# Performance work log

Hardware: AMD Instinct MI355X
Metric: run time of the kernel (lower is better)

## Reference

```python
import jax, jax.numpy as jnp
import numpy as np

N = 8192
D = 256

def setup_inputs() -> dict:
    key = jax.random.key(0)
    k1, k2, k3 = jax.random.split(key, 3)
    x = jax.random.normal(k1, (N, D), dtype=jnp.float32)
    adj_matrix = jax.random.uniform(k2, (N, N), dtype=jnp.float32)
    weight = jax.random.normal(k3, (D, D), dtype=jnp.float32) * 0.02
    bias = jnp.zeros((D,), dtype=jnp.float32)
    return {"x": x, "adj_matrix": adj_matrix, "weight": weight, "bias": bias}

def reference(x, adj_matrix, weight, bias):
    # degree = row sums of adjacency
    degree = jnp.sum(adj_matrix, axis=1)  # [N]
    inv_deg = 1.0 / degree               # inverse of diagonal degree matrix
    # D^-1 @ A @ D^-1 == A scaled by inv_deg on rows and columns
    normalized_adj = adj_matrix * inv_deg[:, None] * inv_deg[None, :]  # [N,N]
    h = jnp.matmul(normalized_adj, x)          # [N,D] aggregation
    h = jnp.matmul(h, weight) + bias           # [N,D] transform
    return jax.nn.relu(h)
```

## Files before the change

kernel.cpp:

```cpp
#include <hip/hip_runtime.h>
#include <stdint.h>
#include <stdio.h>

#define NROWS 8192
#define DDIM 256

typedef __attribute__((ext_vector_type(8))) __bf16 bf16x8;
typedef __attribute__((ext_vector_type(4))) float f32x4;
typedef __attribute__((address_space(3))) uint32_t as3u32;
typedef __attribute__((address_space(1))) uint32_t as1u32;

__device__ __forceinline__ void glds16(const void* g, void* l) {
  __builtin_amdgcn_global_load_lds((const as1u32*)g, (as3u32*)l, 16, 0, 0);
}

__device__ __forceinline__ ushort f2b(float f) {
  uint32_t u = __float_as_uint(f);
  return (ushort)((u + 0x7FFFu + ((u >> 16) & 1u)) >> 16);
}

__global__ __launch_bounds__(256) void degree_cast_kernel(const float* __restrict__ A,
                                                          ushort* __restrict__ Ab,
                                                          float* __restrict__ inv_deg) {
  const int row = blockIdx.x * 4 + (threadIdx.x >> 6);
  const int lane = threadIdx.x & 63;
  const float4* r4 = (const float4*)(A + (size_t)row * NROWS);
  ushort* wr = Ab + (size_t)row * NROWS;
  float s = 0.f;
#pragma unroll
  for (int i = 0; i < 32; ++i) {
    float4 v = r4[lane + (i << 6)];
    s += (v.x + v.y) + (v.z + v.w);
    ushort4 b;
    b.x = f2b(v.x); b.y = f2b(v.y); b.z = f2b(v.z); b.w = f2b(v.w);
    *(ushort4*)(wr + (size_t)(lane + (i << 6)) * 4) = b;
  }
#pragma unroll
  for (int o = 32; o > 0; o >>= 1) s += __shfl_xor(s, o, 64);
  if (lane == 0) inv_deg[row] = 1.0f / s;
}

__global__ __launch_bounds__(256) void transpose_scale_kernel(const float* __restrict__ src,
                                                              const float* __restrict__ scale,
                                                              ushort* __restrict__ dst, int K) {
  __shared__ ushort tile[64 * 256];
  const int k0 = blockIdx.x * 64;
  const int w = threadIdx.x >> 6;
  const int lane = threadIdx.x & 63;
#pragma unroll
  for (int i = 0; i < 16; ++i) {
    const int r = w * 16 + i;
    float4 v = *(const float4*)(src + (size_t)(k0 + r) * DDIM + lane * 4);
    const float sc = scale ? scale[k0 + r] : 1.0f;
    ushort4 b;
    b.x = f2b(v.x * sc); b.y = f2b(v.y * sc);
    b.z = f2b(v.z * sc); b.w = f2b(v.w * sc);
    *(ushort4*)&tile[r * 256 + lane * 4] = b;
  }
  __syncthreads();
  const int c = threadIdx.x;
  ushort* drow = dst + (size_t)c * K + k0;
#pragma unroll
  for (int s = 0; s < 8; ++s) {
    uint32_t p[4];
#pragma unroll
    for (int j = 0; j < 4; ++j) {
      uint32_t lo = tile[(s * 8 + 2 * j + 0) * 256 + c];
      uint32_t hi = tile[(s * 8 + 2 * j + 1) * 256 + c];
      p[j] = lo | (hi << 16);
    }
    uint4 u; u.x = p[0]; u.y = p[1]; u.z = p[2]; u.w = p[3];
    *(uint4*)(drow + s * 8) = u;
  }
}

__global__ __launch_bounds__(512, 2) void gemm_big_kernel(
    const ushort* __restrict__ Ab,
    const ushort* __restrict__ Bt,
    const float* __restrict__ rowscale,
    float* __restrict__ Cpart) {
  __shared__ ushort Asm[2][128 * 64];
  __shared__ ushort Bsm[2][256 * 64];

  const int tid = threadIdx.x;
  const int lane = tid & 63;
  const int w = tid >> 6;
  const int wm = w >> 2;
  const int wn = w & 3;

  const int ks = blockIdx.x & 3;
  const int mb = blockIdx.x >> 2;
  const int m0 = mb * 128;
  const size_t kstart = (size_t)ks * 2048;

  const int al_r = lane >> 3;
  const int al_c = lane & 7;
  const int asw = al_c ^ al_r;
  const char* agA = (const char*)(Ab + (size_t)(m0 + 16 * w + al_r) * NROWS + kstart) + asw * 16;
  const char* bgB = (const char*)(Bt + (size_t)(32 * w + al_r) * NROWS + kstart) + asw * 16;
  const size_t grp = (size_t)8 * NROWS * 2;

  const int fr = lane & 15;
  const int q = lane >> 4;
  const int fsw = fr & 7;

  f32x4 acc[4][4] = {};
  const int NT = 2048 / 64;

  {
    glds16(agA, &Asm[0][(16 * w + 0) * 64]);
    glds16(agA + grp, &Asm[0][(16 * w + 8) * 64]);
#pragma unroll
    for (int j = 0; j < 4; ++j)
      glds16(bgB + (size_t)j * grp, &Bsm[0][(32 * w + 8 * j) * 64]);
  }

  int cur = 0;
  for (int t = 0; t < NT; ++t) {
    __syncthreads();
    if (t + 1 < NT) {
      const size_t koff = (size_t)(t + 1) * 128;
      glds16(agA + koff, &Asm[cur ^ 1][(16 * w + 0) * 64]);
      glds16(agA + grp + koff, &Asm[cur ^ 1][(16 * w + 8) * 64]);
#pragma unroll
      for (int j = 0; j < 4; ++j)
        glds16(bgB + (size_t)j * grp + koff, &Bsm[cur ^ 1][(32 * w + 8 * j) * 64]);
    }
#pragma unroll
    for (int kk = 0; kk < 2; ++kk) {
      uint4 af[4], bfr[4];
#pragma unroll
      for (int m = 0; m < 4; ++m)
        af[m] = *(const uint4*)((const char*)&Asm[cur][0] +
                 ((64 * wm + 16 * m + fr) * 128 + (((4 * kk + q) ^ fsw) << 4)));
#pragma unroll
      for (int n = 0; n < 4; ++n)
        bfr[n] = *(const uint4*)((const char*)&Bsm[cur][0] +
                 ((64 * wn + 16 * n + fr) * 128 + (((4 * kk + q) ^ fsw) << 4)));
#pragma unroll
      for (int m = 0; m < 4; ++m)
#pragma unroll
        for (int n = 0; n < 4; ++n)
          acc[m][n] = __builtin_amdgcn_mfma_f32_16x16x32_bf16(
              __builtin_bit_cast(bf16x8, af[m]), __builtin_bit_cast(bf16x8, bfr[n]),
              acc[m][n], 0, 0, 0);
    }
    cur ^= 1;
  }

  float* Cp = Cpart + (size_t)ks * ((size_t)NROWS * DDIM);
#pragma unroll
  for (int m = 0; m < 4; ++m)
#pragma unroll
    for (int r = 0; r < 4; ++r) {
      const int row = m0 + 64 * wm + 16 * m + q * 4 + r;
      const float sc = rowscale[row];
#pragma unroll
      for (int n = 0; n < 4; ++n) {
        const int col = 64 * wn + 16 * n + fr;
        Cp[(size_t)row * DDIM + col] = acc[m][n][r] * sc;
      }
    }
}

__global__ __launch_bounds__(512, 4) void gemm_small_kernel(
    const float* __restrict__ Hp, int npart, size_t pstride,
    const ushort* __restrict__ Bt,
    const float* __restrict__ bias, float* __restrict__ C) {
  const int K = DDIM;
  __shared__ ushort Asm[2][32 * 32];
  __shared__ ushort Bsm[2][256 * 32];

  const int tid = threadIdx.x;
  const int lane = tid & 63;
  const int w = tid >> 6;
  const int m0 = blockIdx.x * 32;

  f32x4 acc[2][2] = {};
  const int NT = K >> 5;

  const int arow = tid >> 3;
  const int aseg = tid & 7;
  const float* ag = Hp + (size_t)(m0 + arow) * DDIM + aseg * 4;
  const int awoff = arow * 32 + ((((aseg >> 1) ^ ((arow >> 1) & 3)) << 3) | ((aseg & 1) << 2));

  const int bch0 = w * 2;
  const int bq = lane >> 2;
  const int bswz = (lane & 3) ^ ((lane >> 3) & 3);
  const char* bg0 = (const char*)Bt + (size_t)(bch0 * 16 + bq) * ((size_t)K * 2) + bswz * 16;
  const char* bg1 = bg0 + (size_t)16 * ((size_t)K * 2);

  const int fr = lane & 15;
  const int fsw = (fr >> 1) & 3;
  const int fch = (lane >> 4) ^ fsw;
  const int aoff0 = fr * 32 + (fch << 3);
  const int aoff1 = (16 + fr) * 32 + (fch << 3);
  const int boff0 = (w * 32 + fr) * 32 + (fch << 3);
  const int boff1 = (w * 32 + 16 + fr) * 32 + (fch << 3);

  auto loadA = [&](int t) {
    float4 v; v.x = v.y = v.z = v.w = 0.f;
    for (int p = 0; p < npart; ++p) {
      float4 u = *(const float4*)(ag + (size_t)p * pstride + t * 32);
      v.x += u.x; v.y += u.y; v.z += u.z; v.w += u.w;
    }
    return v;
  };

  if (tid < 256) {
    float4 v = loadA(0);
    ushort4 b; b.x = f2b(v.x); b.y = f2b(v.y); b.z = f2b(v.z); b.w = f2b(v.w);
    *(ushort4*)&Asm[0][awoff] = b;
  }
  glds16(bg0, &Bsm[0][(bch0 + 0) * 512]);
  glds16(bg1, &Bsm[0][(bch0 + 1) * 512]);

  int cur = 0;
  for (int t = 0; t < NT; ++t) {
    __syncthreads();
    const bool pf = (t + 1 < NT);
    float4 av;
    if (pf) {
      if (tid < 256) av = loadA(t + 1);
      glds16(bg0 + (size_t)(t + 1) * 64, &Bsm[cur ^ 1][(bch0 + 0) * 512]);
      glds16(bg1 + (size_t)(t + 1) * 64, &Bsm[cur ^ 1][(bch0 + 1) * 512]);
    }
    uint4 a0 = *(const uint4*)&Asm[cur][aoff0];
    uint4 a1 = *(const uint4*)&Asm[cur][aoff1];
    uint4 b0 = *(const uint4*)&Bsm[cur][boff0];
    uint4 b1 = *(const uint4*)&Bsm[cur][boff1];
    acc[0][0] = __builtin_amdgcn_mfma_f32_16x16x32_bf16(
        __builtin_bit_cast(bf16x8, a0), __builtin_bit_cast(bf16x8, b0), acc[0][0], 0, 0, 0);
    acc[0][1] = __builtin_amdgcn_mfma_f32_16x16x32_bf16(
        __builtin_bit_cast(bf16x8, a0), __builtin_bit_cast(bf16x8, b1), acc[0][1], 0, 0, 0);
    acc[1][0] = __builtin_amdgcn_mfma_f32_16x16x32_bf16(
        __builtin_bit_cast(bf16x8, a1), __builtin_bit_cast(bf16x8, b0), acc[1][0], 0, 0, 0);
    acc[1][1] = __builtin_amdgcn_mfma_f32_16x16x32_bf16(
        __builtin_bit_cast(bf16x8, a1), __builtin_bit_cast(bf16x8, b1), acc[1][1], 0, 0, 0);
    if (pf && tid < 256) {
      ushort4 b; b.x = f2b(av.x); b.y = f2b(av.y); b.z = f2b(av.z); b.w = f2b(av.w);
      *(ushort4*)&Asm[cur ^ 1][awoff] = b;
    }
    cur ^= 1;
  }

#pragma unroll
  for (int m = 0; m < 2; ++m)
#pragma unroll
    for (int n = 0; n < 2; ++n) {
      const int col = w * 32 + n * 16 + fr;
      const float bv = bias[col];
#pragma unroll
      for (int r = 0; r < 4; ++r) {
        const int row = m0 + m * 16 + (lane >> 4) * 4 + r;
        float x = acc[m][n][r] + bv;
        x = fmaxf(x, 0.f);
        C[(size_t)row * DDIM + col] = x;
      }
    }
}

extern "C" void kernel_launch(void* const* d_in, const int* in_sizes, int n_in,
                              void* d_out, int out_size, void* d_ws, size_t ws_size,
                              hipStream_t stream) {
  const float* x      = (const float*)d_in[0];
  const float* adj    = (const float*)d_in[1];
  const float* weight = (const float*)d_in[2];
  const float* bias   = (const float*)d_in[3];
  float* out = (float*)d_out;

  char* ws = (char*)d_ws;
  const size_t ab_bytes = (size_t)NROWS * NROWS * 2;
  const size_t h_bytes  = 4ull * NROWS * DDIM * 4;
  const size_t yt_bytes = (size_t)DDIM * NROWS * 2;
  const size_t wt_bytes = (size_t)DDIM * DDIM * 2;
  ushort* Ab      = (ushort*)ws;
  float*  hpart   = (float*)(ws + ab_bytes);
  ushort* Yt      = (ushort*)(ws + ab_bytes + h_bytes);
  ushort* Wt      = (ushort*)(ws + ab_bytes + h_bytes + yt_bytes);
  float*  inv_deg = (float*)(ws + ab_bytes + h_bytes + yt_bytes + wt_bytes);
  const size_t need = ab_bytes + h_bytes + yt_bytes + wt_bytes + (size_t)NROWS * 4;
  if (ws_size < need) { fprintf(stderr, "ws too small: %zu < %zu\n", ws_size, need); return; }

  degree_cast_kernel<<<NROWS / 4, 256, 0, stream>>>(adj, Ab, inv_deg);
  transpose_scale_kernel<<<NROWS / 64, 256, 0, stream>>>(x, inv_deg, Yt, NROWS);
  transpose_scale_kernel<<<DDIM / 64, 256, 0, stream>>>(weight, nullptr, Wt, DDIM);
  gemm_big_kernel<<<dim3(256), 512, 0, stream>>>(Ab, Yt, inv_deg, hpart);
  gemm_small_kernel<<<dim3(256), 512, 0, stream>>>(hpart, 4, (size_t)NROWS * DDIM, Wt, bias, out);
}
```

Measured before the change: 472.1 us.

## Shrink big GEMM tile to 64 rows with 4 waves and unroll partial-sum loads

The big aggregation GEMM now uses 64-row M tiles, 256 threads (4 waves, each owning 64 output columns) and twice as many blocks (512), so every CU gets more blocks and the work is spread more evenly. Each block now loads the full 256-column B tile for only 64 rows of A, which lowers B reuse and raises global traffic for B per unit of output. The small GEMM hardcodes the 4 split-K partials and loads all of them at once, then sums them in a tree, giving more memory-level parallelism.

```diff
diff --git a/kernel.cpp b/kernel.cpp
--- a/kernel.cpp
+++ b/kernel.cpp
@@ -74,30 +74,28 @@
   }
 }
 
-__global__ __launch_bounds__(512, 2) void gemm_big_kernel(
+__global__ __launch_bounds__(256, 2) void gemm_big_kernel(
     const ushort* __restrict__ Ab,
     const ushort* __restrict__ Bt,
     const float* __restrict__ rowscale,
     float* __restrict__ Cpart) {
-  __shared__ ushort Asm[2][128 * 64];
+  __shared__ ushort Asm[2][64 * 64];
   __shared__ ushort Bsm[2][256 * 64];
 
   const int tid = threadIdx.x;
   const int lane = tid & 63;
   const int w = tid >> 6;
-  const int wm = w >> 2;
-  const int wn = w & 3;
 
   const int ks = blockIdx.x & 3;
   const int mb = blockIdx.x >> 2;
-  const int m0 = mb * 128;
+  const int m0 = mb * 64;
   const size_t kstart = (size_t)ks * 2048;
 
   const int al_r = lane >> 3;
   const int al_c = lane & 7;
   const int asw = al_c ^ al_r;
   const char* agA = (const char*)(Ab + (size_t)(m0 + 16 * w + al_r) * NROWS + kstart) + asw * 16;
-  const char* bgB = (const char*)(Bt + (size_t)(32 * w + al_r) * NROWS + kstart) + asw * 16;
+  const char* bgB = (const char*)(Bt + (size_t)(64 * w + al_r) * NROWS + kstart) + asw * 16;
   const size_t grp = (size_t)8 * NROWS * 2;
 
   const int fr = lane & 15;
@@ -107,36 +105,31 @@
   f32x4 acc[4][4] = {};
   const int NT = 2048 / 64;
 
-  {
-    glds16(agA, &Asm[0][(16 * w + 0) * 64]);
-    glds16(agA + grp, &Asm[0][(16 * w + 8) * 64]);
-#pragma unroll
-    for (int j = 0; j < 4; ++j)
-      glds16(bgB + (size_t)j * grp, &Bsm[0][(32 * w + 8 * j) * 64]);
-  }
-
+  auto stage = [&](int buf, int t) {
+    const size_t koff = (size_t)t * 128;
+    glds16(agA + koff, &Asm[buf][(16 * w + 0) * 64]);
+    glds16(agA + grp + koff, &Asm[buf][(16 * w + 8) * 64]);
+#pragma unroll
+    for (int j = 0; j < 8; ++j)
+      glds16(bgB + (size_t)j * grp + koff, &Bsm[buf][(64 * w + 8 * j) * 64]);
+  };
+
+  stage(0, 0);
   int cur = 0;
   for (int t = 0; t < NT; ++t) {
     __syncthreads();
-    if (t + 1 < NT) {
-      const size_t koff = (size_t)(t + 1) * 128;
-      glds16(agA + koff, &Asm[cur ^ 1][(16 * w + 0) * 64]);
-      glds16(agA + grp + koff, &Asm[cur ^ 1][(16 * w + 8) * 64]);
-#pragma unroll
-      for (int j = 0; j < 4; ++j)
-        glds16(bgB + (size_t)j * grp + koff, &Bsm[cur ^ 1][(32 * w + 8 * j) * 64]);
-    }
+    if (t + 1 < NT) stage(cur ^ 1, t + 1);
 #pragma unroll
     for (int kk = 0; kk < 2; ++kk) {
       uint4 af[4], bfr[4];
 #pragma unroll
       for (int m = 0; m < 4; ++m)
         af[m] = *(const uint4*)((const char*)&Asm[cur][0] +
-                 ((64 * wm + 16 * m + fr) * 128 + (((4 * kk + q) ^ fsw) << 4)));
+                 ((16 * m + fr) * 128 + (((4 * kk + q) ^ fsw) << 4)));
 #pragma unroll
       for (int n = 0; n < 4; ++n)
         bfr[n] = *(const uint4*)((const char*)&Bsm[cur][0] +
-                 ((64 * wn + 16 * n + fr) * 128 + (((4 * kk + q) ^ fsw) << 4)));
+                 ((64 * w + 16 * n + fr) * 128 + (((4 * kk + q) ^ fsw) << 4)));
 #pragma unroll
       for (int m = 0; m < 4; ++m)
 #pragma unroll
@@ -153,21 +146,22 @@
   for (int m = 0; m < 4; ++m)
 #pragma unroll
     for (int r = 0; r < 4; ++r) {
-      const int row = m0 + 64 * wm + 16 * m + q * 4 + r;
+      const int row = m0 + 16 * m + q * 4 + r;
       const float sc = rowscale[row];
 #pragma unroll
       for (int n = 0; n < 4; ++n) {
-        const int col = 64 * wn + 16 * n + fr;
+        const int col = 64 * w + 16 * n + fr;
         Cp[(size_t)row * DDIM + col] = acc[m][n][r] * sc;
       }
     }
 }
 
 __global__ __launch_bounds__(512, 4) void gemm_small_kernel(
-    const float* __restrict__ Hp, int npart, size_t pstride,
+    const float* __restrict__ Hp,
     const ushort* __restrict__ Bt,
     const float* __restrict__ bias, float* __restrict__ C) {
   const int K = DDIM;
+  const size_t PS = (size_t)NROWS * DDIM;
   __shared__ ushort Asm[2][32 * 32];
   __shared__ ushort Bsm[2][256 * 32];
 
@@ -199,11 +193,15 @@
   const int boff1 = (w * 32 + 16 + fr) * 32 + (fch << 3);
 
   auto loadA = [&](int t) {
-    float4 v; v.x = v.y = v.z = v.w = 0.f;
-    for (int p = 0; p < npart; ++p) {
-      float4 u = *(const float4*)(ag + (size_t)p * pstride + t * 32);
-      v.x += u.x; v.y += u.y; v.z += u.z; v.w += u.w;
-    }
+    float4 u0 = *(const float4*)(ag + 0 * PS + t * 32);
+    float4 u1 = *(const float4*)(ag + 1 * PS + t * 32);
+    float4 u2 = *(const float4*)(ag + 2 * PS + t * 32);
+    float4 u3 = *(const float4*)(ag + 3 * PS + t * 32);
+    float4 v;
+    v.x = (u0.x + u1.x) + (u2.x + u3.x);
+    v.y = (u0.y + u1.y) + (u2.y + u3.y);
+    v.z = (u0.z + u1.z) + (u2.z + u3.z);
+    v.w = (u0.w + u1.w) + (u2.w + u3.w);
     return v;
   };
 
@@ -285,6 +283,6 @@
   degree_cast_kernel<<<NROWS / 4, 256, 0, stream>>>(adj, Ab, inv_deg);
   transpose_scale_kernel<<<NROWS / 64, 256, 0, stream>>>(x, inv_deg, Yt, NROWS);
   transpose_scale_kernel<<<DDIM / 64, 256, 0, stream>>>(weight, nullptr, Wt, DDIM);
-  gemm_big_kernel<<<dim3(256), 512, 0, stream>>>(Ab, Yt, inv_deg, hpart);
-  gemm_small_kernel<<<dim3(256), 512, 0, stream>>>(hpart, 4, (size_t)NROWS * DDIM, Wt, bias, out);
-}
+  gemm_big_kernel<<<dim3(512), 256, 0, stream>>>(Ab, Yt, inv_deg, hpart);
+  gemm_small_kernel<<<dim3(256), 512, 0, stream>>>(hpart, Wt, bias, out);
+}
```

Result: no change. 463.8 us (-1.8%).
